# Kernel tuning notes

Hardware: AMD Instinct MI355X
Metric: run time of the kernel (lower is better)

The kernel has to match this reference:

```python
import jax, jax.numpy as jnp
import numpy as np

EPS = 1e-12  # F.normalize eps


def _sage(x, k, w_l, b_l, w_r):
    # Faithful to the source's edge_index bug: directed edges i->j (i<j) among
    # global nodes 0..k-1 only (duplicated batch_size times, which leaves the
    # mean unchanged). agg[j] = mean_{i<j} x[i] for j<k; 0 for j>=k (PyG
    # scatter-mean yields 0 for nodes with no in-edges).
    xk = x[:k]                                    # [k, d_in]
    csum = jnp.cumsum(xk, axis=0)                 # [k, d_in]
    prev = jnp.concatenate([jnp.zeros_like(xk[:1]), csum[:-1]], axis=0)
    cnt = jnp.arange(k, dtype=x.dtype)[:, None]   # node j has j in-neighbors
    agg_k = prev / jnp.maximum(cnt, 1.0)          # [k, d_in]
    agg = jnp.zeros_like(x).at[:k].set(agg_k)     # [N, d_in]
    # PyG SAGEConv: out = lin_l(aggr) + lin_r(x); bias lives in lin_l
    out = agg @ w_l.T + b_l + x @ w_r.T           # [N, d_out]
    nrm = jnp.linalg.norm(out, axis=-1, keepdims=True)
    return out / jnp.maximum(nrm, EPS)


def setup_inputs() -> dict:
    key = jax.random.key(0)
    B, K = 32, 1024
    P, I, R = 1024, 128, 256  # problem_size, intermediate_size, rnn_size
    ks = jax.random.split(key, 13)
    dims = [(P, I), (I, 2 * I), (2 * I, I), (I, R)]
    inp = {"flow_matrix": jax.random.normal(ks[0], (B, K, K), dtype=jnp.float32)}
    for li, (din, dout) in enumerate(dims, start=1):
        s = 1.0 / np.sqrt(din)
        inp[f"w_l{li}"] = jax.random.uniform(ks[3 * li - 2], (dout, din), jnp.float32, -s, s)
        inp[f"b_l{li}"] = jax.random.uniform(ks[3 * li - 1], (dout,), jnp.float32, -s, s)
        inp[f"w_r{li}"] = jax.random.uniform(ks[3 * li], (dout, din), jnp.float32, -s, s)
    return inp


def reference(flow_matrix, w_l1, b_l1, w_r1, w_l2, b_l2, w_r2,
              w_l3, b_l3, w_r3, w_l4, b_l4, w_r4):
    B, K, P = flow_matrix.shape
    x = flow_matrix.reshape(-1, P)               # [B*K, P]
    x = _sage(x, K, w_l1, b_l1, w_r1)
    x = _sage(x, K, w_l2, b_l2, w_r2)
    x = _sage(x, K, w_l3, b_l3, w_r3)
    x = _sage(x, K, w_l4, b_l4, w_r4)
    x = jax.nn.relu(x)
    return (x.reshape(B, K, -1), 1)
```

## Files before the change

kernel.cpp:

```cpp
#include <hip/hip_runtime.h>
#include <math.h>


typedef __attribute__((ext_vector_type(8))) short short8;
typedef __attribute__((ext_vector_type(4))) float f32x4;

constexpr int NROWS = 32768;
constexpr int KROWS = 1024;

static __device__ __forceinline__ unsigned short f2bf(float f) {
    unsigned int u = __float_as_uint(f);
    return (unsigned short)((u + 0x7fffu + ((u >> 16) & 1u)) >> 16);
}

template<int ROWS>
struct RegsBF {
    short8 v[ROWS / 32];
    __device__ __forceinline__ void load(const unsigned short* src, int ld,
                                         int r0, int k0, int t) {
#pragma unroll
        for (int j = 0; j < ROWS / 32; ++j) {
            int idx = j * 256 + t; int r = idx >> 3, f = idx & 7;
            v[j] = *reinterpret_cast<const short8*>(
                src + (size_t)(r0 + r) * ld + k0 + f * 8);
        }
    }
    __device__ __forceinline__ void store(unsigned short* buf, int t) {
#pragma unroll
        for (int j = 0; j < ROWS / 32; ++j) {
            int idx = j * 256 + t; int r = idx >> 3, f = idx & 7;
            int off = (r * 128 + f * 16) ^ ((r & 7) << 4);
            *reinterpret_cast<short8*>((char*)buf + off) = v[j];
        }
    }
};

template<int ROWS>
struct RegsF32 {
    float4 v[ROWS / 16];
    __device__ __forceinline__ void load(const float* src, int ld,
                                         int r0, int k0, int t) {
#pragma unroll
        for (int j = 0; j < ROWS / 32; ++j) {
            int idx = j * 256 + t; int r = idx >> 3, f = idx & 7;
            const float* p = src + (size_t)(r0 + r) * ld + k0 + f * 8;
            v[2 * j]     = *reinterpret_cast<const float4*>(p);
            v[2 * j + 1] = *reinterpret_cast<const float4*>(p + 4);
        }
    }
    __device__ __forceinline__ void store(unsigned short* buf, int t) {
#pragma unroll
        for (int j = 0; j < ROWS / 32; ++j) {
            int idx = j * 256 + t; int r = idx >> 3, f = idx & 7;
            float4 a = v[2 * j], b = v[2 * j + 1];
            short8 s;
            s[0] = (short)f2bf(a.x); s[1] = (short)f2bf(a.y);
            s[2] = (short)f2bf(a.z); s[3] = (short)f2bf(a.w);
            s[4] = (short)f2bf(b.x); s[5] = (short)f2bf(b.y);
            s[6] = (short)f2bf(b.z); s[7] = (short)f2bf(b.w);
            int off = (r * 128 + f * 16) ^ ((r & 7) << 4);
            *reinterpret_cast<short8*>((char*)buf + off) = s;
        }
    }
};

template<int DIN, int DOUT, bool AFP32, bool BFP32>
__device__ __forceinline__ void proj_dbuf(const void* __restrict__ Xv,
    const void* __restrict__ Wv, unsigned short* __restrict__ YT, int i0, int t,
    unsigned short* Ab0, unsigned short* Ab1,
    unsigned short* Bb0, unsigned short* Bb1)
{
    constexpr int WN = DOUT / 64, WM = 4 / WN, FM = DOUT / 128, NT = DIN / 64;
    const int wv = t >> 6, lane = t & 63, wr_ = wv / WN, wc = wv % WN;
    f32x4 acc[FM][4];
#pragma unroll
    for (int fi = 0; fi < FM; ++fi)
#pragma unroll
        for (int fj = 0; fj < 4; ++fj) acc[fi][fj] = (f32x4){0.f, 0.f, 0.f, 0.f};

    RegsF32<32>  arf; RegsBF<32>  arb;
    RegsF32<DOUT> brf; RegsBF<DOUT> brb;
    if (AFP32) arf.load((const float*)Xv, DIN, i0, 0, t);
    else       arb.load((const unsigned short*)Xv, DIN, i0, 0, t);
    if (BFP32) brf.load((const float*)Wv, DIN, 0, 0, t);
    else       brb.load((const unsigned short*)Wv, DIN, 0, 0, t);
    if (AFP32) arf.store(Ab0, t); else arb.store(Ab0, t);
    if (BFP32) brf.store(Bb0, t); else brb.store(Bb0, t);
    if (NT > 1) {
        if (AFP32) arf.load((const float*)Xv, DIN, i0, 64, t);
        else       arb.load((const unsigned short*)Xv, DIN, i0, 64, t);
        if (BFP32) brf.load((const float*)Wv, DIN, 0, 64, t);
        else       brb.load((const unsigned short*)Wv, DIN, 0, 64, t);
    }
    __syncthreads();

    for (int kt = 0; kt < NT; ++kt) {
        const unsigned short* Ac = (kt & 1) ? Ab1 : Ab0;
        const unsigned short* Bc = (kt & 1) ? Bb1 : Bb0;
#pragma unroll
        for (int kk = 0; kk < 2; ++kk) {
            short8 a[FM], b[4];
#pragma unroll
            for (int fi = 0; fi < FM; ++fi) {
                const int rA = wr_ * (32 / WM) + fi * 16 + (lane & 15);
                const int off = (rA * 128 + kk * 64 + (lane >> 4) * 16) ^ ((rA & 7) << 4);
                a[fi] = *reinterpret_cast<const short8*>((const char*)Ac + off);
            }
#pragma unroll
            for (int fj = 0; fj < 4; ++fj) {
                const int rB = wc * 64 + fj * 16 + (lane & 15);
                const int off = (rB * 128 + kk * 64 + (lane >> 4) * 16) ^ ((rB & 7) << 4);
                b[fj] = *reinterpret_cast<const short8*>((const char*)Bc + off);
            }
#pragma unroll
            for (int fi = 0; fi < FM; ++fi)
#pragma unroll
                for (int fj = 0; fj < 4; ++fj)
                    acc[fi][fj] = __builtin_amdgcn_mfma_f32_16x16x32_bf16(
                        a[fi], b[fj], acc[fi][fj], 0, 0, 0);
        }
        if (kt + 1 < NT) {
            unsigned short* An = (kt & 1) ? Ab0 : Ab1;
            unsigned short* Bn = (kt & 1) ? Bb0 : Bb1;
            if (AFP32) arf.store(An, t); else arb.store(An, t);
            if (BFP32) brf.store(Bn, t); else brb.store(Bn, t);
            if (kt + 2 < NT) {
                const int kn = (kt + 2) * 64;
                if (AFP32) arf.load((const float*)Xv, DIN, i0, kn, t);
                else       arb.load((const unsigned short*)Xv, DIN, i0, kn, t);
                if (BFP32) brf.load((const float*)Wv, DIN, 0, kn, t);
                else       brb.load((const unsigned short*)Wv, DIN, 0, kn, t);
            }
        }
        __syncthreads();
    }
#pragma unroll
    for (int fi = 0; fi < FM; ++fi)
#pragma unroll
        for (int fj = 0; fj < 4; ++fj) {
            const int rl0 = wr_ * (32 / WM) + fi * 16 + ((lane >> 4) << 2);
            const int cl  = wc * 64 + fj * 16 + (lane & 15);
            ushort4 y;
            y.x = f2bf(acc[fi][fj][0]); y.y = f2bf(acc[fi][fj][1]);
            y.z = f2bf(acc[fi][fj][2]); y.w = f2bf(acc[fi][fj][3]);
            *reinterpret_cast<ushort4*>(YT + (size_t)cl * KROWS + i0 + rl0) = y;
        }
}

__global__ __launch_bounds__(256, 2)
void prep_kernel(const float* __restrict__ flow, const float* __restrict__ wl1,
                 const float* __restrict__ wr1, const float* __restrict__ wl2,
                 const float* __restrict__ wr2, const float* __restrict__ wl3,
                 const float* __restrict__ wr3, const float* __restrict__ wl4,
                 const float* __restrict__ wr4,
                 unsigned short* __restrict__ wbf,
                 unsigned short* __restrict__ YT1, float* __restrict__ outscalar)
{
    __shared__ unsigned short Ab0[32 * 64], Ab1[32 * 64];
    __shared__ unsigned short Bb0[128 * 64], Bb1[128 * 64];
    const int t = threadIdx.x, bid = blockIdx.x;
    if (bid >= 32) {
        if (bid == 32 && t == 0) outscalar[0] = 1.0f;
        int g = (bid - 32) * 1024 + t * 4;
        const float* src; int off;
        if      (g < 131072) { src = wr1; off = g; }
        else if (g < 163840) { src = wl2; off = g - 131072; }
        else if (g < 196608) { src = wr2; off = g - 163840; }
        else if (g < 229376) { src = wl3; off = g - 196608; }
        else if (g < 262144) { src = wr3; off = g - 229376; }
        else if (g < 294912) { src = wl4; off = g - 262144; }
        else                 { src = wr4; off = g - 294912; }
        float4 v = *reinterpret_cast<const float4*>(src + off);
        ushort4 o4;
        o4.x = f2bf(v.x); o4.y = f2bf(v.y); o4.z = f2bf(v.z); o4.w = f2bf(v.w);
        *reinterpret_cast<ushort4*>(wbf + g) = o4;
        return;
    }
    proj_dbuf<1024, 128, true, true>(flow, wl1, YT1, bid * 32, t,
                                     Ab0, Ab1, Bb0, Bb1);
}

template<int DIN, int DOUT>
__global__ __launch_bounds__(256, 2)
void proj_kernel(const unsigned short* __restrict__ X,
                 const unsigned short* __restrict__ W,
                 unsigned short* __restrict__ YT)
{
    __shared__ unsigned short Ab0[32 * 64], Ab1[32 * 64];
    __shared__ unsigned short Bb0[DOUT * 64], Bb1[DOUT * 64];
    proj_dbuf<DIN, DOUT, false, false>(X, W, YT, blockIdx.x * 32, threadIdx.x,
                                       Ab0, Ab1, Bb0, Bb1);
}

template<int DOUT, int BM, int WM, int WN, int MODE, bool AFP32, int MINW>
__global__ __launch_bounds__(256, MINW)
void mfma_gemm(const void* __restrict__ Xv,
               const unsigned short* __restrict__ W,
               const float* __restrict__ bias,
               const unsigned short* __restrict__ YT,
               float* __restrict__ outf,
               unsigned short* __restrict__ outb,
               int din)
{
    constexpr int BN = WN * 64;
    static_assert(BN == DOUT, "block must own full output rows");
    constexpr int FM = BM / (WM * 16);
    __shared__ unsigned short Abuf[BM * 64];
    __shared__ unsigned short Bbuf[BN * 64];
    __shared__ float ssred[WN * BM];

    const int t = threadIdx.x, wvid = t >> 6, lane = t & 63;
    const int wr_ = wvid / WN, wc = wvid % WN;
    const int i0 = blockIdx.x * BM;
    const int nt = din >> 6;
    const bool hasagg = (i0 < KROWS);

    f32x4 agg[FM][4];
#pragma unroll
    for (int fi = 0; fi < FM; ++fi)
#pragma unroll
        for (int fj = 0; fj < 4; ++fj) agg[fi][fj] = (f32x4){0.f, 0.f, 0.f, 0.f};

    if (hasagg) {
        const int nt2 = (i0 + BM + 63) >> 6;
        RegsBF<BN> sb;
        sb.load(YT, KROWS, 0, 0, t);
        for (int kt = 0; kt < nt2; ++kt) {
            if (kt) __syncthreads();
            sb.store(Bbuf, t);
            __syncthreads();
            if (kt + 1 < nt2) sb.load(YT, KROWS, 0, (kt + 1) * 64, t);
#pragma unroll
            for (int kk = 0; kk < 2; ++kk) {
                const int jb = kt * 64 + kk * 32 + ((lane >> 4) << 3);
                short8 a[FM], b[4];
#pragma unroll
                for (int fi = 0; fi < FM; ++fi) {
                    const int irow = i0 + wr_ * (BM / WM) + fi * 16 + (lane & 15);
#pragma unroll
                    for (int e = 0; e < 8; ++e)
                        a[fi][e] = (short)((jb + e < irow) ? 0x3F80 : 0);
                }
#pragma unroll
                for (int fj = 0; fj < 4; ++fj) {
                    int rB = wc * 64 + fj * 16 + (lane & 15);
                    int off = (rB * 128 + kk * 64 + (lane >> 4) * 16) ^ ((rB & 7) << 4);
                    b[fj] = *reinterpret_cast<const short8*>((const char*)Bbuf + off);
                }
#pragma unroll
                for (int fi = 0; fi < FM; ++fi)
#pragma unroll
                    for (int fj = 0; fj < 4; ++fj)
                        agg[fi][fj] = __builtin_amdgcn_mfma_f32_16x16x32_bf16(
                            a[fi], b[fj], agg[fi][fj], 0, 0, 0);
            }
        }
#pragma unroll
        for (int fi = 0; fi < FM; ++fi)
#pragma unroll
            for (int reg = 0; reg < 4; ++reg) {
                int i_abs = i0 + wr_ * (BM / WM) + fi * 16 + ((lane >> 4) << 2) + reg;
                float inv = 1.0f / (float)(i_abs > 1 ? i_abs : 1);
#pragma unroll
                for (int fj = 0; fj < 4; ++fj) agg[fi][fj][reg] *= inv;
            }
        __syncthreads();
    }

    f32x4 acc[FM][4];
#pragma unroll
    for (int fi = 0; fi < FM; ++fi)
#pragma unroll
        for (int fj = 0; fj < 4; ++fj) acc[fi][fj] = (f32x4){0.f, 0.f, 0.f, 0.f};

    RegsBF<BN> brg;
    RegsF32<BM> arf;
    RegsBF<BM> arb;
    if (AFP32) arf.load((const float*)Xv, din, i0, 0, t);
    else       arb.load((const unsigned short*)Xv, din, i0, 0, t);
    brg.load(W, din, 0, 0, t);

    for (int kt = 0; kt < nt; ++kt) {
        if (kt) __syncthreads();
        if (AFP32) arf.store(Abuf, t); else arb.store(Abuf, t);
        brg.store(Bbuf, t);
        __syncthreads();
        if (kt + 1 < nt) {
            int kn = (kt + 1) * 64;
            if (AFP32) arf.load((const float*)Xv, din, i0, kn, t);
            else       arb.load((const unsigned short*)Xv, din, i0, kn, t);
            brg.load(W, din, 0, kn, t);
        }
#pragma unroll
        for (int kk = 0; kk < 2; ++kk) {
            short8 a[FM], b[4];
#pragma unroll
            for (int fi = 0; fi < FM; ++fi) {
                int rA = wr_ * (BM / WM) + fi * 16 + (lane & 15);
                int off = (rA * 128 + kk * 64 + (lane >> 4) * 16) ^ ((rA & 7) << 4);
                a[fi] = *reinterpret_cast<const short8*>((const char*)Abuf + off);
            }
#pragma unroll
            for (int fj = 0; fj < 4; ++fj) {
                int rB = wc * 64 + fj * 16 + (lane & 15);
                int off = (rB * 128 + kk * 64 + (lane >> 4) * 16) ^ ((rB & 7) << 4);
                b[fj] = *reinterpret_cast<const short8*>((const char*)Bbuf + off);
            }
#pragma unroll
            for (int fi = 0; fi < FM; ++fi)
#pragma unroll
                for (int fj = 0; fj < 4; ++fj)
                    acc[fi][fj] = __builtin_amdgcn_mfma_f32_16x16x32_bf16(
                        a[fi], b[fj], acc[fi][fj], 0, 0, 0);
        }
    }

    float bb[4];
#pragma unroll
    for (int fj = 0; fj < 4; ++fj) bb[fj] = bias[wc * 64 + fj * 16 + (lane & 15)];

#pragma unroll
    for (int fi = 0; fi < FM; ++fi)
#pragma unroll
        for (int fj = 0; fj < 4; ++fj)
#pragma unroll
            for (int reg = 0; reg < 4; ++reg)
                acc[fi][fj][reg] += bb[fj] + agg[fi][fj][reg];

    float sstot[FM][4];
#pragma unroll
    for (int fi = 0; fi < FM; ++fi)
#pragma unroll
        for (int reg = 0; reg < 4; ++reg) {
            float s = 0.f;
#pragma unroll
            for (int fj = 0; fj < 4; ++fj) {
                float v = acc[fi][fj][reg];
                s += v * v;
            }
#pragma unroll
            for (int m = 8; m >= 1; m >>= 1) s += __shfl_xor(s, m);
            if ((lane & 15) == 0) {
                int rl = wr_ * (BM / WM) + fi * 16 + ((lane >> 4) << 2) + reg;
                ssred[wc * BM + rl] = s;
            }
        }
    __syncthreads();
#pragma unroll
    for (int fi = 0; fi < FM; ++fi)
#pragma unroll
        for (int reg = 0; reg < 4; ++reg) {
            int rl = wr_ * (BM / WM) + fi * 16 + ((lane >> 4) << 2) + reg;
            float s = 0.f;
#pragma unroll
            for (int c = 0; c < WN; ++c) s += ssred[c * BM + rl];
            sstot[fi][reg] = 1.0f / fmaxf(sqrtf(s), 1e-12f);
        }

#pragma unroll
    for (int fi = 0; fi < FM; ++fi)
#pragma unroll
        for (int fj = 0; fj < 4; ++fj)
#pragma unroll
            for (int reg = 0; reg < 4; ++reg) {
                int rl = wr_ * (BM / WM) + fi * 16 + ((lane >> 4) << 2) + reg;
                int cl = wc * 64 + fj * 16 + (lane & 15);
                float v = acc[fi][fj][reg] * sstot[fi][reg];
                if (MODE == 2) {
                    v = fmaxf(v, 0.f);
                    outf[(size_t)(i0 + rl) * DOUT + cl] = v;
                } else {
                    outb[(size_t)(i0 + rl) * DOUT + cl] = f2bf(v);
                }
            }
}

extern "C" void kernel_launch(void* const* d_in, const int* in_sizes, int n_in,
                              void* d_out, int out_size, void* d_ws, size_t ws_size,
                              hipStream_t stream)
{
    const float* flow = (const float*)d_in[0];
    const float* wl1 = (const float*)d_in[1];
    const float* bl1 = (const float*)d_in[2];
    const float* wr1 = (const float*)d_in[3];
    const float* wl2 = (const float*)d_in[4];
    const float* bl2 = (const float*)d_in[5];
    const float* wr2 = (const float*)d_in[6];
    const float* wl3 = (const float*)d_in[7];
    const float* bl3 = (const float*)d_in[8];
    const float* wr3 = (const float*)d_in[9];
    const float* wl4 = (const float*)d_in[10];
    const float* bl4 = (const float*)d_in[11];
    const float* wr4 = (const float*)d_in[12];
    float* out = (float*)d_out;

    char* p = (char*)d_ws;
    unsigned short* wbf = (unsigned short*)p;  p += 1 << 20;
    unsigned short* xA  = (unsigned short*)p;  p += (size_t)NROWS * 128 * 2;
    unsigned short* xB  = (unsigned short*)p;  p += (size_t)NROWS * 256 * 2;
    unsigned short* YT1 = (unsigned short*)p;  p += (size_t)128 * KROWS * 2;
    unsigned short* YT2 = (unsigned short*)p;  p += (size_t)256 * KROWS * 2;
    unsigned short* YT3 = (unsigned short*)p;  p += (size_t)128 * KROWS * 2;
    unsigned short* YT4 = (unsigned short*)p;

    const unsigned short* wr1b = wbf;
    const unsigned short* wl2b = wbf + 131072;
    const unsigned short* wr2b = wbf + 163840;
    const unsigned short* wl3b = wbf + 196608;
    const unsigned short* wr3b = wbf + 229376;
    const unsigned short* wl4b = wbf + 262144;
    const unsigned short* wr4b = wbf + 294912;

    prep_kernel<<<352, 256, 0, stream>>>(flow, wl1, wr1, wl2, wr2, wl3, wr3,
                                         wl4, wr4, wbf, YT1,
                                         out + (size_t)NROWS * 256);
    mfma_gemm<128, 32, 2, 2, 1, true , 4><<<1024, 256, 0, stream>>>(
        flow, wr1b, bl1, YT1, nullptr, xA, 1024);
    proj_kernel<128, 256><<<32, 256, 0, stream>>>(xA, wl2b, YT2);
    mfma_gemm<256, 32, 1, 4, 1, false, 3><<<1024, 256, 0, stream>>>(
        xA, wr2b, bl2, YT2, nullptr, xB, 128);
    proj_kernel<256, 128><<<32, 256, 0, stream>>>(xB, wl3b, YT3);
    mfma_gemm<128, 32, 2, 2, 1, false, 4><<<1024, 256, 0, stream>>>(
        xB, wr3b, bl3, YT3, nullptr, xA, 256);
    proj_kernel<128, 256><<<32, 256, 0, stream>>>(xA, wl4b, YT4);
    mfma_gemm<256, 32, 1, 4, 2, false, 3><<<1024, 256, 0, stream>>>(
        xA, wr4b, bl4, YT4, out, nullptr, 128);
}
```

Baseline: 112.7 us.

## Replace triangular prefix-sum MFMA with per-tile column sums plus local triangle

The projection kernels now also write per-32-row column sums (T buffers) of the projected features. The gemm kernels build the prefix aggregate by summing these tile totals for all preceding tiles and applying a single masked 64-wide triangular MFMA for the local part, instead of looping over all earlier 64-row tiles with MFMAs. This removes the O(i0) MFMA and shared-memory staging work in the aggregation of blocks covering the first 1024 rows. In exchange it adds a block-level reduction and sync in the projection kernels and summation in fp32 from tile sums, which slightly changes rounding.

```diff
diff --git a/kernel.cpp b/kernel.cpp
--- a/kernel.cpp
+++ b/kernel.cpp
@@ -64,11 +64,41 @@
     }
 };
 
+template<int BM, int WM, int WN, int FM>
+__device__ __forceinline__ void mfma_tile(const unsigned short* Abuf,
+    const unsigned short* Bbuf, f32x4 (&acc)[FM][4], int wr_, int wc, int lane)
+{
+#pragma unroll
+    for (int kk = 0; kk < 2; ++kk) {
+        short8 a[FM], b[4];
+#pragma unroll
+        for (int fi = 0; fi < FM; ++fi) {
+            const int rA = wr_ * (BM / WM) + fi * 16 + (lane & 15);
+            const int off = (rA * 128 + kk * 64 + (lane >> 4) * 16) ^ ((rA & 7) << 4);
+            a[fi] = *reinterpret_cast<const short8*>((const char*)Abuf + off);
+        }
+#pragma unroll
+        for (int fj = 0; fj < 4; ++fj) {
+            const int rB = wc * 64 + fj * 16 + (lane & 15);
+            const int off = (rB * 128 + kk * 64 + (lane >> 4) * 16) ^ ((rB & 7) << 4);
+            b[fj] = *reinterpret_cast<const short8*>((const char*)Bbuf + off);
+        }
+#pragma unroll
+        for (int fi = 0; fi < FM; ++fi)
+#pragma unroll
+            for (int fj = 0; fj < 4; ++fj)
+                acc[fi][fj] = __builtin_amdgcn_mfma_f32_16x16x32_bf16(
+                    a[fi], b[fj], acc[fi][fj], 0, 0, 0);
+    }
+}
+
 template<int DIN, int DOUT, bool AFP32, bool BFP32>
 __device__ __forceinline__ void proj_dbuf(const void* __restrict__ Xv,
-    const void* __restrict__ Wv, unsigned short* __restrict__ YT, int i0, int t,
+    const void* __restrict__ Wv, unsigned short* __restrict__ YT,
+    float* __restrict__ Tg,
+    int i0, int t,
     unsigned short* Ab0, unsigned short* Ab1,
-    unsigned short* Bb0, unsigned short* Bb1)
+    unsigned short* Bb0, unsigned short* Bb1, float* Tred)
 {
     constexpr int WN = DOUT / 64, WM = 4 / WN, FM = DOUT / 128, NT = DIN / 64;
     const int wv = t >> 6, lane = t & 63, wr_ = wv / WN, wc = wv % WN;
@@ -97,28 +127,7 @@
     for (int kt = 0; kt < NT; ++kt) {
         const unsigned short* Ac = (kt & 1) ? Ab1 : Ab0;
         const unsigned short* Bc = (kt & 1) ? Bb1 : Bb0;
-#pragma unroll
-        for (int kk = 0; kk < 2; ++kk) {
-            short8 a[FM], b[4];
-#pragma unroll
-            for (int fi = 0; fi < FM; ++fi) {
-                const int rA = wr_ * (32 / WM) + fi * 16 + (lane & 15);
-                const int off = (rA * 128 + kk * 64 + (lane >> 4) * 16) ^ ((rA & 7) << 4);
-                a[fi] = *reinterpret_cast<const short8*>((const char*)Ac + off);
-            }
-#pragma unroll
-            for (int fj = 0; fj < 4; ++fj) {
-                const int rB = wc * 64 + fj * 16 + (lane & 15);
-                const int off = (rB * 128 + kk * 64 + (lane >> 4) * 16) ^ ((rB & 7) << 4);
-                b[fj] = *reinterpret_cast<const short8*>((const char*)Bc + off);
-            }
-#pragma unroll
-            for (int fi = 0; fi < FM; ++fi)
-#pragma unroll
-                for (int fj = 0; fj < 4; ++fj)
-                    acc[fi][fj] = __builtin_amdgcn_mfma_f32_16x16x32_bf16(
-                        a[fi], b[fj], acc[fi][fj], 0, 0, 0);
-        }
+        mfma_tile<32, WM, WN, FM>(Ac, Bc, acc, wr_, wc, lane);
         if (kt + 1 < NT) {
             unsigned short* An = (kt & 1) ? Ab0 : Ab1;
             unsigned short* Bn = (kt & 1) ? Bb0 : Bb1;
@@ -145,6 +154,31 @@
             y.z = f2bf(acc[fi][fj][2]); y.w = f2bf(acc[fi][fj][3]);
             *reinterpret_cast<ushort4*>(YT + (size_t)cl * KROWS + i0 + rl0) = y;
         }
+    {
+        float v[4];
+#pragma unroll
+        for (int fj = 0; fj < 4; ++fj) {
+            float s = 0.f;
+#pragma unroll
+            for (int fi = 0; fi < FM; ++fi)
+#pragma unroll
+                for (int reg = 0; reg < 4; ++reg) s += acc[fi][fj][reg];
+            s += __shfl_xor(s, 16);
+            s += __shfl_xor(s, 32);
+            v[fj] = s;
+        }
+        if (lane < 16) {
+#pragma unroll
+            for (int fj = 0; fj < 4; ++fj)
+                Tred[wr_ * DOUT + wc * 64 + fj * 16 + lane] = v[fj];
+        }
+        __syncthreads();
+        if (t < DOUT) {
+            float s = Tred[t];
+            if constexpr (WM == 2) s += Tred[DOUT + t];
+            Tg[t] = s;
+        }
+    }
 }
 
 __global__ __launch_bounds__(256, 2)
@@ -154,10 +188,12 @@
                  const float* __restrict__ wr3, const float* __restrict__ wl4,
                  const float* __restrict__ wr4,
                  unsigned short* __restrict__ wbf,
-                 unsigned short* __restrict__ YT1, float* __restrict__ outscalar)
+                 unsigned short* __restrict__ YT1, float* __restrict__ T1,
+                 float* __restrict__ outscalar)
 {
     __shared__ unsigned short Ab0[32 * 64], Ab1[32 * 64];
     __shared__ unsigned short Bb0[128 * 64], Bb1[128 * 64];
+    __shared__ float Tred[256];
     const int t = threadIdx.x, bid = blockIdx.x;
     if (bid >= 32) {
         if (bid == 32 && t == 0) outscalar[0] = 1.0f;
@@ -176,20 +212,22 @@
         *reinterpret_cast<ushort4*>(wbf + g) = o4;
         return;
     }
-    proj_dbuf<1024, 128, true, true>(flow, wl1, YT1, bid * 32, t,
-                                     Ab0, Ab1, Bb0, Bb1);
+    proj_dbuf<1024, 128, true, true>(flow, wl1, YT1, T1 + bid * 128,
+                                     bid * 32, t, Ab0, Ab1, Bb0, Bb1, Tred);
 }
 
 template<int DIN, int DOUT>
 __global__ __launch_bounds__(256, 2)
 void proj_kernel(const unsigned short* __restrict__ X,
                  const unsigned short* __restrict__ W,
-                 unsigned short* __restrict__ YT)
+                 unsigned short* __restrict__ YT, float* __restrict__ T)
 {
     __shared__ unsigned short Ab0[32 * 64], Ab1[32 * 64];
     __shared__ unsigned short Bb0[DOUT * 64], Bb1[DOUT * 64];
-    proj_dbuf<DIN, DOUT, false, false>(X, W, YT, blockIdx.x * 32, threadIdx.x,
-                                       Ab0, Ab1, Bb0, Bb1);
+    __shared__ float Tred[256];
+    proj_dbuf<DIN, DOUT, false, false>(X, W, YT, T + blockIdx.x * DOUT,
+                                       blockIdx.x * 32, threadIdx.x,
+                                       Ab0, Ab1, Bb0, Bb1, Tred);
 }
 
 template<int DOUT, int BM, int WM, int WN, int MODE, bool AFP32, int MINW>
@@ -198,6 +236,7 @@
                const unsigned short* __restrict__ W,
                const float* __restrict__ bias,
                const unsigned short* __restrict__ YT,
+               const float* __restrict__ Tbuf,
                float* __restrict__ outf,
                unsigned short* __restrict__ outb,
                int din)
@@ -221,48 +260,67 @@
 #pragma unroll
         for (int fj = 0; fj < 4; ++fj) agg[fi][fj] = (f32x4){0.f, 0.f, 0.f, 0.f};
 
+    float Pv[4] = {0.f, 0.f, 0.f, 0.f};
     if (hasagg) {
-        const int nt2 = (i0 + BM + 63) >> 6;
+        const int m = i0 >> 5;
+        const int colb = wc * 64 + (lane & 15);
+        float Pa[4] = {0.f, 0.f, 0.f, 0.f};
+        int mp = 0;
+        for (; mp + 1 < m; mp += 2) {
+            const float* T0 = Tbuf + (size_t)mp * DOUT + colb;
+            const float* T1 = T0 + DOUT;
+#pragma unroll
+            for (int fj = 0; fj < 4; ++fj) {
+                Pv[fj] += T0[fj * 16];
+                Pa[fj] += T1[fj * 16];
+            }
+        }
+        if (mp < m) {
+            const float* T0 = Tbuf + (size_t)mp * DOUT + colb;
+#pragma unroll
+            for (int fj = 0; fj < 4; ++fj) Pv[fj] += T0[fj * 16];
+        }
+#pragma unroll
+        for (int fj = 0; fj < 4; ++fj) Pv[fj] += Pa[fj];
+
+        const int base = i0 & ~63;
         RegsBF<BN> sb;
-        sb.load(YT, KROWS, 0, 0, t);
-        for (int kt = 0; kt < nt2; ++kt) {
-            if (kt) __syncthreads();
-            sb.store(Bbuf, t);
-            __syncthreads();
-            if (kt + 1 < nt2) sb.load(YT, KROWS, 0, (kt + 1) * 64, t);
-#pragma unroll
-            for (int kk = 0; kk < 2; ++kk) {
-                const int jb = kt * 64 + kk * 32 + ((lane >> 4) << 3);
-                short8 a[FM], b[4];
-#pragma unroll
-                for (int fi = 0; fi < FM; ++fi) {
-                    const int irow = i0 + wr_ * (BM / WM) + fi * 16 + (lane & 15);
-#pragma unroll
-                    for (int e = 0; e < 8; ++e)
-                        a[fi][e] = (short)((jb + e < irow) ? 0x3F80 : 0);
-                }
-#pragma unroll
-                for (int fj = 0; fj < 4; ++fj) {
-                    int rB = wc * 64 + fj * 16 + (lane & 15);
-                    int off = (rB * 128 + kk * 64 + (lane >> 4) * 16) ^ ((rB & 7) << 4);
-                    b[fj] = *reinterpret_cast<const short8*>((const char*)Bbuf + off);
-                }
-#pragma unroll
-                for (int fi = 0; fi < FM; ++fi)
-#pragma unroll
-                    for (int fj = 0; fj < 4; ++fj)
-                        agg[fi][fj] = __builtin_amdgcn_mfma_f32_16x16x32_bf16(
-                            a[fi], b[fj], agg[fi][fj], 0, 0, 0);
-            }
+        sb.load(YT, KROWS, 0, base, t);
+        sb.store(Bbuf, t);
+        __syncthreads();
+#pragma unroll
+        for (int kk = 0; kk < 2; ++kk) {
+            const int jb = base + kk * 32 + ((lane >> 4) << 3);
+            short8 a[FM], b[4];
+#pragma unroll
+            for (int fi = 0; fi < FM; ++fi) {
+                const int irow = i0 + wr_ * (BM / WM) + fi * 16 + (lane & 15);
+#pragma unroll
+                for (int e = 0; e < 8; ++e)
+                    a[fi][e] = (short)((jb + e >= i0 && jb + e < irow) ? 0x3F80 : 0);
+            }
+#pragma unroll
+            for (int fj = 0; fj < 4; ++fj) {
+                const int rB = wc * 64 + fj * 16 + (lane & 15);
+                const int off = (rB * 128 + kk * 64 + (lane >> 4) * 16) ^ ((rB & 7) << 4);
+                b[fj] = *reinterpret_cast<const short8*>((const char*)Bbuf + off);
+            }
+#pragma unroll
+            for (int fi = 0; fi < FM; ++fi)
+#pragma unroll
+                for (int fj = 0; fj < 4; ++fj)
+                    agg[fi][fj] = __builtin_amdgcn_mfma_f32_16x16x32_bf16(
+                        a[fi], b[fj], agg[fi][fj], 0, 0, 0);
         }
 #pragma unroll
         for (int fi = 0; fi < FM; ++fi)
 #pragma unroll
             for (int reg = 0; reg < 4; ++reg) {
-                int i_abs = i0 + wr_ * (BM / WM) + fi * 16 + ((lane >> 4) << 2) + reg;
-                float inv = 1.0f / (float)(i_abs > 1 ? i_abs : 1);
-#pragma unroll
-                for (int fj = 0; fj < 4; ++fj) agg[fi][fj][reg] *= inv;
+                const int i_abs = i0 + wr_ * (BM / WM) + fi * 16 + ((lane >> 4) << 2) + reg;
+                const float inv = 1.0f / (float)(i_abs > 1 ? i_abs : 1);
+#pragma unroll
+                for (int fj = 0; fj < 4; ++fj)
+                    agg[fi][fj][reg] = (agg[fi][fj][reg] + Pv[fj]) * inv;
             }
         __syncthreads();
     }
@@ -291,28 +349,7 @@
             else       arb.load((const unsigned short*)Xv, din, i0, kn, t);
             brg.load(W, din, 0, kn, t);
         }
-#pragma unroll
-        for (int kk = 0; kk < 2; ++kk) {
-            short8 a[FM], b[4];
-#pragma unroll
-            for (int fi = 0; fi < FM; ++fi) {
-                int rA = wr_ * (BM / WM) + fi * 16 + (lane & 15);
-                int off = (rA * 128 + kk * 64 + (lane >> 4) * 16) ^ ((rA & 7) << 4);
-                a[fi] = *reinterpret_cast<const short8*>((const char*)Abuf + off);
-            }
-#pragma unroll
-            for (int fj = 0; fj < 4; ++fj) {
-                int rB = wc * 64 + fj * 16 + (lane & 15);
-                int off = (rB * 128 + kk * 64 + (lane >> 4) * 16) ^ ((rB & 7) << 4);
-                b[fj] = *reinterpret_cast<const short8*>((const char*)Bbuf + off);
-            }
-#pragma unroll
-            for (int fi = 0; fi < FM; ++fi)
-#pragma unroll
-                for (int fj = 0; fj < 4; ++fj)
-                    acc[fi][fj] = __builtin_amdgcn_mfma_f32_16x16x32_bf16(
-                        a[fi], b[fj], acc[fi][fj], 0, 0, 0);
-        }
+        mfma_tile<BM, WM, WN, FM>(Abuf, Bbuf, acc, wr_, wc, lane);
     }
 
     float bb[4];
@@ -339,7 +376,7 @@
                 s += v * v;
             }
 #pragma unroll
-            for (int m = 8; m >= 1; m >>= 1) s += __shfl_xor(s, m);
+            for (int m2 = 8; m2 >= 1; m2 >>= 1) s += __shfl_xor(s, m2);
             if ((lane & 15) == 0) {
                 int rl = wr_ * (BM / WM) + fi * 16 + ((lane >> 4) << 2) + reg;
                 ssred[wc * BM + rl] = s;
@@ -401,7 +438,11 @@
     unsigned short* YT1 = (unsigned short*)p;  p += (size_t)128 * KROWS * 2;
     unsigned short* YT2 = (unsigned short*)p;  p += (size_t)256 * KROWS * 2;
     unsigned short* YT3 = (unsigned short*)p;  p += (size_t)128 * KROWS * 2;
-    unsigned short* YT4 = (unsigned short*)p;
+    unsigned short* YT4 = (unsigned short*)p;  p += (size_t)256 * KROWS * 2;
+    float* T1 = (float*)p;                     p += (size_t)32 * 128 * 4;
+    float* T2 = (float*)p;                     p += (size_t)32 * 256 * 4;
+    float* T3 = (float*)p;                     p += (size_t)32 * 128 * 4;
+    float* T4 = (float*)p;
 
     const unsigned short* wr1b = wbf;
     const unsigned short* wl2b = wbf + 131072;
@@ -412,17 +453,17 @@
     const unsigned short* wr4b = wbf + 294912;
 
     prep_kernel<<<352, 256, 0, stream>>>(flow, wl1, wr1, wl2, wr2, wl3, wr3,
-                                         wl4, wr4, wbf, YT1,
+                                         wl4, wr4, wbf, YT1, T1,
                                          out + (size_t)NROWS * 256);
     mfma_gemm<128, 32, 2, 2, 1, true , 4><<<1024, 256, 0, stream>>>(
-        flow, wr1b, bl1, YT1, nullptr, xA, 1024);
-    proj_kernel<128, 256><<<32, 256, 0, stream>>>(xA, wl2b, YT2);
+        flow, wr1b, bl1, YT1, T1, nullptr, xA, 1024);
+    proj_kernel<128, 256><<<32, 256, 0, stream>>>(xA, wl2b, YT2, T2);
     mfma_gemm<256, 32, 1, 4, 1, false, 3><<<1024, 256, 0, stream>>>(
-        xA, wr2b, bl2, YT2, nullptr, xB, 128);
-    proj_kernel<256, 128><<<32, 256, 0, stream>>>(xB, wl3b, YT3);
+        xA, wr2b, bl2, YT2, T2, nullptr, xB, 128);
+    proj_kernel<256, 128><<<32, 256, 0, stream>>>(xB, wl3b, YT3, T3);
     mfma_gemm<128, 32, 2, 2, 1, false, 4><<<1024, 256, 0, stream>>>(
-        xB, wr3b, bl3, YT3, nullptr, xA, 256);
-    proj_kernel<128, 256><<<32, 256, 0, stream>>>(xA, wl4b, YT4);
+        xB, wr3b, bl3, YT3, T3, nullptr, xA, 256);
+    proj_kernel<128, 256><<<32, 256, 0, stream>>>(xA, wl4b, YT4, T4);
     mfma_gemm<256, 32, 1, 4, 2, false, 3><<<1024, 256, 0, stream>>>(
-        xA, wr4b, bl4, YT4, out, nullptr, 128);
-}
+        xA, wr4b, bl4, YT4, T4, out, nullptr, 128);
+}
```

Measured after the change: 94.54 us. -16.1%, faster.
